# Kernel optimization log

Hardware: AMD Instinct MI355X
Metric: run time of the kernel (lower is better)

Reference implementation:

```python
import jax, jax.numpy as jnp
import numpy as np

N = 32768
D = 512          # query_dim = key_dim = value_dim
H = 8            # num_heads


def setup_inputs() -> dict:
    key = jax.random.key(0)
    ks = jax.random.split(key, 8)
    s = 0.02
    return {
        "queries": jax.random.normal(ks[0], (N, D), dtype=jnp.float32),
        "keys": jax.random.normal(ks[1], (N, D), dtype=jnp.float32),
        "values": jax.random.normal(ks[2], (N, D), dtype=jnp.float32),
        # Linear weights stored as [in, out] (torch stores [out, in]; math identical)
        "Wq": jax.random.normal(ks[3], (D, D * H), dtype=jnp.float32) * s,
        "Wk": jax.random.normal(ks[4], (D, D * H), dtype=jnp.float32) * s,
        "Wv": jax.random.normal(ks[5], (D, D * H), dtype=jnp.float32) * s,
        "Wo": jax.random.normal(ks[6], (D * H, D), dtype=jnp.float32) * s,
        "bo": jax.random.normal(ks[7], (D,), dtype=jnp.float32) * s,
    }


def reference(queries, keys, values, Wq, Wk, Wv, Wo, bo):
    # Projections: [N, D] -> [N, H, D]
    Q = (queries @ Wq).reshape(-1, H, D)
    K = (keys @ Wk).reshape(-1, H, D)
    V = (values @ Wv).reshape(-1, H, D)
    # Per-token attention across the HEADS axis (faithful to torch.bmm on [N,H,D])
    attn = jnp.einsum("nhd,ngd->nhg", Q, K)      # [N, H, H], no 1/sqrt(d) scaling
    attn = jax.nn.softmax(attn, axis=-1)
    out = jnp.einsum("nhg,ngd->nhd", attn, V)    # [N, H, D]
    out = out.reshape(-1, H * D)
    return out @ Wo + bo                           # [N, D]
```

## Files before the change

### kernel.cpp

```cpp
#include <hip/hip_runtime.h>
#include <hip/hip_bf16.h>
#include <cstdint>


typedef unsigned short u16;
typedef unsigned int u32;
typedef __bf16 bf16x8 __attribute__((ext_vector_type(8)));
typedef float f32x4 __attribute__((ext_vector_type(4)));

#define DEVI __device__ __forceinline__

DEVI float b2f(u16 u) {
    union { u32 i; float f; } c; c.i = ((u32)u) << 16; return c.f;
}
DEVI u16 f2b(float f) {
    union { float f; u32 i; } c; c.f = f;
    return (u16)((c.i + 0x7FFFu + ((c.i >> 16) & 1u)) >> 16);
}

DEVI void async16(const u16* g, u16* l) {
    __builtin_amdgcn_global_load_lds(
        (const __attribute__((address_space(1))) u32*)g,
        (__attribute__((address_space(3))) u32*)l, 16, 0, 0);
}


__global__ __launch_bounds__(256) void cvt_bf16(const float* __restrict__ in,
                                                u16* __restrict__ out) {
    const int i = blockIdx.x * 256 + threadIdx.x;
    const float4 a = ((const float4*)in)[2 * i];
    const float4 b = ((const float4*)in)[2 * i + 1];
    union { u16 u[8]; uint4 v; } r;
    r.u[0] = f2b(a.x); r.u[1] = f2b(a.y); r.u[2] = f2b(a.z); r.u[3] = f2b(a.w);
    r.u[4] = f2b(b.x); r.u[5] = f2b(b.y); r.u[6] = f2b(b.z); r.u[7] = f2b(b.w);
    ((uint4*)out)[i] = r.v;
}

__global__ void transpose_cvt(const float* __restrict__ in, u16* __restrict__ out,
                              int R, int C) {
    __shared__ float tile[32][33];
    const int c0 = blockIdx.x * 32, r0 = blockIdx.y * 32;
    const int x = threadIdx.x, y = threadIdx.y;
#pragma unroll
    for (int i = 0; i < 4; ++i) {
        const int r = y + i * 8;
        tile[x][r] = in[(long)(r0 + r) * C + c0 + x];
    }
    __syncthreads();
#pragma unroll
    for (int i = 0; i < 4; ++i) {
        const int c = y + i * 8;
        out[(long)(c0 + c) * R + r0 + x] = f2b(tile[c][x]);
    }
}


template <int F32OUT>
__global__ __launch_bounds__(256) void gemm_bt(
    const u16* __restrict__ A, const u16* __restrict__ BT,
    void* __restrict__ Cv, const float* __restrict__ bias,
    int M, int N, int K) {
    __shared__ u16 As[128 * 32];
    __shared__ u16 Bs[128 * 32];
    const int tid = threadIdx.x;
    const int wave = tid >> 6, lane = tid & 63;
    const long row0 = (long)blockIdx.y * 128, col0 = (long)blockIdx.x * 128;
    const int wm = (wave >> 1) * 64, wn = (wave & 1) * 64;
    const int mrow = lane & 15, quad = lane >> 4;

    f32x4 acc[4][4] = {};

    const u16* pA = A + (row0 + wave * 32 + (lane >> 2)) * (long)K + (lane & 3) * 8;
    const u16* pB = BT + (col0 + wave * 32 + (lane >> 2)) * (long)K + (lane & 3) * 8;
    u16* lA = As + wave * 32 * 32;
    u16* lB = Bs + wave * 32 * 32;
    const long skip = 16 * (long)K;

    for (int k0 = 0; k0 < K; k0 += 32) {
        __syncthreads();
        async16(pA, lA);
        async16(pA + skip, lA + 16 * 32);
        async16(pB, lB);
        async16(pB + skip, lB + 16 * 32);
        pA += 32; pB += 32;
        __syncthreads();
        bf16x8 af[4], bfr[4];
#pragma unroll
        for (int i = 0; i < 4; ++i)
            af[i] = *(const bf16x8*)(As + (wm + i * 16 + mrow) * 32 + quad * 8);
#pragma unroll
        for (int j = 0; j < 4; ++j)
            bfr[j] = *(const bf16x8*)(Bs + (wn + j * 16 + mrow) * 32 + quad * 8);
#pragma unroll
        for (int i = 0; i < 4; ++i)
#pragma unroll
            for (int j = 0; j < 4; ++j)
                acc[i][j] = __builtin_amdgcn_mfma_f32_16x16x32_bf16(
                    af[i], bfr[j], acc[i][j], 0, 0, 0);
    }

#pragma unroll
    for (int i = 0; i < 4; ++i) {
        const long r = row0 + wm + i * 16 + quad * 4;
#pragma unroll
        for (int j = 0; j < 4; ++j) {
            const long c = col0 + wn + j * 16 + mrow;
            if (F32OUT) {
                float* C = (float*)Cv;
                const float bv = bias[c];
#pragma unroll
                for (int rr = 0; rr < 4; ++rr)
                    C[(r + rr) * (long)N + c] = acc[i][j][rr] + bv;
            } else {
                u16* C = (u16*)Cv;
#pragma unroll
                for (int rr = 0; rr < 4; ++rr)
                    C[(r + rr) * (long)N + c] = f2b(acc[i][j][rr]);
            }
        }
    }
}


__global__ __launch_bounds__(256) void attn_kernel(
    const u16* __restrict__ Qg, const u16* __restrict__ Kg,
    const u16* __restrict__ Vg, u16* __restrict__ Og) {
    __shared__ uint4 sQ[512], sK[512], sV[512];
    __shared__ float part[4][64];
    __shared__ float logitS[64];
    __shared__ float probS[64];
    const int t = threadIdx.x;
    const long base = (long)blockIdx.x * 4096;

    const uint4* q4 = (const uint4*)(Qg + base);
    const uint4* k4 = (const uint4*)(Kg + base);
    const uint4* v4 = (const uint4*)(Vg + base);
    sQ[t] = q4[t]; sQ[t + 256] = q4[t + 256];
    sK[t] = k4[t]; sK[t + 256] = k4[t + 256];
    sV[t] = v4[t]; sV[t + 256] = v4[t + 256];
    __syncthreads();

    const u16* Qs = (const u16*)sQ;
    const u16* Ks = (const u16*)sK;
    const u16* Vs = (const u16*)sV;

    {
        const int pr = t & 63, ch = t >> 6;
        const int h = pr >> 3, g = pr & 7;
        const u16* qp = Qs + h * 512 + ch * 128;
        const u16* kp = Ks + g * 512 + ch * 128;
        float s = 0.f;
#pragma unroll
        for (int i = 0; i < 128; ++i) s += b2f(qp[i]) * b2f(kp[i]);
        part[ch][pr] = s;
    }
    __syncthreads();
    if (t < 64) logitS[t] = part[0][t] + part[1][t] + part[2][t] + part[3][t];
    __syncthreads();
    if (t < 8) {
        float m = logitS[t * 8];
#pragma unroll
        for (int g = 1; g < 8; ++g) m = fmaxf(m, logitS[t * 8 + g]);
        float e[8], sum = 0.f;
#pragma unroll
        for (int g = 0; g < 8; ++g) { e[g] = __expf(logitS[t * 8 + g] - m); sum += e[g]; }
        const float inv = 1.f / sum;
#pragma unroll
        for (int g = 0; g < 8; ++g) probS[t * 8 + g] = e[g] * inv;
    }
    __syncthreads();

    const int hh = t >> 5, d0 = (t & 31) * 16;
    float p[8];
#pragma unroll
    for (int g = 0; g < 8; ++g) p[g] = probS[hh * 8 + g];
    float o[16];
#pragma unroll
    for (int j = 0; j < 16; ++j) o[j] = 0.f;
#pragma unroll
    for (int g = 0; g < 8; ++g) {
        const u16* vp = Vs + g * 512 + d0;
#pragma unroll
        for (int j = 0; j < 16; ++j) o[j] += p[g] * b2f(vp[j]);
    }
    union { u16 u[16]; uint4 v[2]; } ob;
#pragma unroll
    for (int j = 0; j < 16; ++j) ob.u[j] = f2b(o[j]);
    uint4* op = (uint4*)(Og + base + hh * 512 + d0);
    op[0] = ob.v[0]; op[1] = ob.v[1];
}


extern "C" void kernel_launch(void* const* d_in, const int* in_sizes, int n_in,
                              void* d_out, int out_size, void* d_ws, size_t ws_size,
                              hipStream_t stream) {
    const float* Xq = (const float*)d_in[0];
    const float* Xk = (const float*)d_in[1];
    const float* Xv = (const float*)d_in[2];
    const float* Wq = (const float*)d_in[3];
    const float* Wk = (const float*)d_in[4];
    const float* Wv = (const float*)d_in[5];
    const float* Wo = (const float*)d_in[6];
    const float* bo = (const float*)d_in[7];

    const int N = 32768;
    const size_t FIXED = 16777216ull;
    int Mc = N;
    while (Mc > 128 && FIXED + (size_t)Mc * 27648ull > ws_size) Mc >>= 1;
    if (FIXED + (size_t)Mc * 27648ull > ws_size) return;

    char* ws = (char*)d_ws;
    u16* WqT = (u16*)(ws);
    u16* WkT = (u16*)(ws + 4194304ull);
    u16* WvT = (u16*)(ws + 8388608ull);
    u16* WoT = (u16*)(ws + 12582912ull);
    u16* Xqb = (u16*)(ws + FIXED);
    u16* Xkb = Xqb + (size_t)Mc * 512;
    u16* Xvb = Xkb + (size_t)Mc * 512;
    u16* Qc  = Xvb + (size_t)Mc * 512;
    u16* Kc  = Qc + (size_t)Mc * 4096;
    u16* Vc  = Kc + (size_t)Mc * 4096;

    dim3 tb(32, 8);
    transpose_cvt<<<dim3(128, 16), tb, 0, stream>>>(Wq, WqT, 512, 4096);
    transpose_cvt<<<dim3(128, 16), tb, 0, stream>>>(Wk, WkT, 512, 4096);
    transpose_cvt<<<dim3(128, 16), tb, 0, stream>>>(Wv, WvT, 512, 4096);
    transpose_cvt<<<dim3(16, 128), tb, 0, stream>>>(Wo, WoT, 4096, 512);

    const dim3 gProj(4096 / 128, Mc / 128);
    const dim3 gOut(512 / 128, Mc / 128);
    for (int m0 = 0; m0 < N; m0 += Mc) {
        const long xoff = (long)m0 * 512;
        cvt_bf16<<<Mc / 4, 256, 0, stream>>>(Xq + xoff, Xqb);
        cvt_bf16<<<Mc / 4, 256, 0, stream>>>(Xk + xoff, Xkb);
        cvt_bf16<<<Mc / 4, 256, 0, stream>>>(Xv + xoff, Xvb);
        gemm_bt<0><<<gProj, 256, 0, stream>>>(Xqb, WqT, Qc, nullptr, Mc, 4096, 512);
        gemm_bt<0><<<gProj, 256, 0, stream>>>(Xkb, WkT, Kc, nullptr, Mc, 4096, 512);
        gemm_bt<0><<<gProj, 256, 0, stream>>>(Xvb, WvT, Vc, nullptr, Mc, 4096, 512);
        attn_kernel<<<Mc, 256, 0, stream>>>(Qc, Kc, Vc, Qc);
        gemm_bt<1><<<gOut, 256, 0, stream>>>(Qc, WoT, (float*)d_out + xoff, bo,
                                             Mc, 512, 4096);
    }
}
```

Measured before the change: 1.536 ms.

## Double-buffer GEMM LDS tiles, batch QKV projections, and swizzle blocks across XCDs

The GEMM kernel now keeps two LDS buffers and prefetches the next K-slice while MFMAs run on the current one, replacing the load-then-barrier pattern with one barrier per iteration. The three Q/K/V projection GEMMs are merged into a single launch using blockIdx.z and strided operand pointers, with the converted inputs and transposed weights laid out contiguously. Block indices are also remapped so that neighbouring tiles land on the same XCD, for better L2 reuse. LDS use per block doubles, which may lower occupancy, and the pipeline depends on the barrier waiting for the async LDS loads to finish.

```diff
diff --git a/kernel.cpp b/kernel.cpp
--- a/kernel.cpp
+++ b/kernel.cpp
@@ -57,14 +57,28 @@
 
 template <int F32OUT>
 __global__ __launch_bounds__(256) void gemm_bt(
-    const u16* __restrict__ A, const u16* __restrict__ BT,
+    const u16* __restrict__ Ab, const u16* __restrict__ Bb,
     void* __restrict__ Cv, const float* __restrict__ bias,
-    int M, int N, int K) {
-    __shared__ u16 As[128 * 32];
-    __shared__ u16 Bs[128 * 32];
+    int M, int N, int K, long sAz, long sBz, long sCz) {
+    __shared__ u16 As[2 * 4096];
+    __shared__ u16 Bs[2 * 4096];
     const int tid = threadIdx.x;
     const int wave = tid >> 6, lane = tid & 63;
-    const long row0 = (long)blockIdx.y * 128, col0 = (long)blockIdx.x * 128;
+    const int z = blockIdx.z;
+    const u16* A = Ab + (long)z * sAz;
+    const u16* BT = Bb + (long)z * sBz;
+
+    int bx, by;
+    {
+        const int b = blockIdx.y * gridDim.x + blockIdx.x;
+        if ((gridDim.x & 7) == 0) {
+            const int cb = gridDim.x >> 3;
+            const int xcd = b & 7, j = b >> 3;
+            bx = xcd * cb + (j % cb);
+            by = j / cb;
+        } else { bx = blockIdx.x; by = blockIdx.y; }
+    }
+    const long row0 = (long)by * 128, col0 = (long)bx * 128;
     const int wm = (wave >> 1) * 64, wn = (wave & 1) * 64;
     const int mrow = lane & 15, quad = lane >> 4;
 
@@ -72,25 +86,35 @@
 
     const u16* pA = A + (row0 + wave * 32 + (lane >> 2)) * (long)K + (lane & 3) * 8;
     const u16* pB = BT + (col0 + wave * 32 + (lane >> 2)) * (long)K + (lane & 3) * 8;
-    u16* lA = As + wave * 32 * 32;
-    u16* lB = Bs + wave * 32 * 32;
+    u16* lA = As + wave * 1024;
+    u16* lB = Bs + wave * 1024;
     const long skip = 16 * (long)K;
 
+    async16(pA, lA);
+    async16(pA + skip, lA + 512);
+    async16(pB, lB);
+    async16(pB + skip, lB + 512);
+
     for (int k0 = 0; k0 < K; k0 += 32) {
+        const int cur = (k0 >> 5) & 1;
         __syncthreads();
-        async16(pA, lA);
-        async16(pA + skip, lA + 16 * 32);
-        async16(pB, lB);
-        async16(pB + skip, lB + 16 * 32);
-        pA += 32; pB += 32;
-        __syncthreads();
+        if (k0 + 32 < K) {
+            const int nb = (cur ^ 1) * 4096;
+            const long o = k0 + 32;
+            async16(pA + o, lA + nb);
+            async16(pA + o + skip, lA + nb + 512);
+            async16(pB + o, lB + nb);
+            async16(pB + o + skip, lB + nb + 512);
+        }
+        const u16* sA = As + cur * 4096;
+        const u16* sB = Bs + cur * 4096;
         bf16x8 af[4], bfr[4];
 #pragma unroll
         for (int i = 0; i < 4; ++i)
-            af[i] = *(const bf16x8*)(As + (wm + i * 16 + mrow) * 32 + quad * 8);
+            af[i] = *(const bf16x8*)(sA + (wm + i * 16 + mrow) * 32 + quad * 8);
 #pragma unroll
         for (int j = 0; j < 4; ++j)
-            bfr[j] = *(const bf16x8*)(Bs + (wn + j * 16 + mrow) * 32 + quad * 8);
+            bfr[j] = *(const bf16x8*)(sB + (wn + j * 16 + mrow) * 32 + quad * 8);
 #pragma unroll
         for (int i = 0; i < 4; ++i)
 #pragma unroll
@@ -106,13 +130,13 @@
         for (int j = 0; j < 4; ++j) {
             const long c = col0 + wn + j * 16 + mrow;
             if (F32OUT) {
-                float* C = (float*)Cv;
+                float* C = (float*)Cv + (long)z * sCz;
                 const float bv = bias[c];
 #pragma unroll
                 for (int rr = 0; rr < 4; ++rr)
                     C[(r + rr) * (long)N + c] = acc[i][j][rr] + bv;
             } else {
-                u16* C = (u16*)Cv;
+                u16* C = (u16*)Cv + (long)z * sCz;
 #pragma unroll
                 for (int rr = 0; rr < 4; ++rr)
                     C[(r + rr) * (long)N + c] = f2b(acc[i][j][rr]);
@@ -211,34 +235,31 @@
 
     char* ws = (char*)d_ws;
     u16* WqT = (u16*)(ws);
-    u16* WkT = (u16*)(ws + 4194304ull);
-    u16* WvT = (u16*)(ws + 8388608ull);
     u16* WoT = (u16*)(ws + 12582912ull);
     u16* Xqb = (u16*)(ws + FIXED);
-    u16* Xkb = Xqb + (size_t)Mc * 512;
-    u16* Xvb = Xkb + (size_t)Mc * 512;
-    u16* Qc  = Xvb + (size_t)Mc * 512;
+    u16* Qc  = Xqb + (size_t)3 * Mc * 512;
     u16* Kc  = Qc + (size_t)Mc * 4096;
     u16* Vc  = Kc + (size_t)Mc * 4096;
 
     dim3 tb(32, 8);
     transpose_cvt<<<dim3(128, 16), tb, 0, stream>>>(Wq, WqT, 512, 4096);
-    transpose_cvt<<<dim3(128, 16), tb, 0, stream>>>(Wk, WkT, 512, 4096);
-    transpose_cvt<<<dim3(128, 16), tb, 0, stream>>>(Wv, WvT, 512, 4096);
+    transpose_cvt<<<dim3(128, 16), tb, 0, stream>>>(Wk, WqT + 2097152, 512, 4096);
+    transpose_cvt<<<dim3(128, 16), tb, 0, stream>>>(Wv, WqT + 4194304, 512, 4096);
     transpose_cvt<<<dim3(16, 128), tb, 0, stream>>>(Wo, WoT, 4096, 512);
 
-    const dim3 gProj(4096 / 128, Mc / 128);
-    const dim3 gOut(512 / 128, Mc / 128);
+    const dim3 gProj(4096 / 128, Mc / 128, 3);
+    const dim3 gOut(512 / 128, Mc / 128, 1);
     for (int m0 = 0; m0 < N; m0 += Mc) {
         const long xoff = (long)m0 * 512;
         cvt_bf16<<<Mc / 4, 256, 0, stream>>>(Xq + xoff, Xqb);
-        cvt_bf16<<<Mc / 4, 256, 0, stream>>>(Xk + xoff, Xkb);
-        cvt_bf16<<<Mc / 4, 256, 0, stream>>>(Xv + xoff, Xvb);
-        gemm_bt<0><<<gProj, 256, 0, stream>>>(Xqb, WqT, Qc, nullptr, Mc, 4096, 512);
-        gemm_bt<0><<<gProj, 256, 0, stream>>>(Xkb, WkT, Kc, nullptr, Mc, 4096, 512);
-        gemm_bt<0><<<gProj, 256, 0, stream>>>(Xvb, WvT, Vc, nullptr, Mc, 4096, 512);
+        cvt_bf16<<<Mc / 4, 256, 0, stream>>>(Xk + xoff, Xqb + (size_t)Mc * 512);
+        cvt_bf16<<<Mc / 4, 256, 0, stream>>>(Xv + xoff, Xqb + (size_t)2 * Mc * 512);
+        gemm_bt<0><<<gProj, 256, 0, stream>>>(Xqb, WqT, Qc, nullptr,
+                                              Mc, 4096, 512,
+                                              (long)Mc * 512, 2097152L,
+                                              (long)Mc * 4096);
         attn_kernel<<<Mc, 256, 0, stream>>>(Qc, Kc, Vc, Qc);
         gemm_bt<1><<<gOut, 256, 0, stream>>>(Qc, WoT, (float*)d_out + xoff, bo,
-                                             Mc, 512, 4096);
-    }
-}
+                                             Mc, 512, 4096, 0L, 0L, 0L);
+    }
+}
```

After: 1.422 ms. -7.5%, faster.
